# Optimization experiments

Hardware: AMD Instinct MI355X
Metric: run time of the kernel (lower is better)

The kernel has to match this reference:

```python
import jax, jax.numpy as jnp
import numpy as np

N, D, E, NNZ = 200000, 128, 1024, 1600000


def setup_inputs() -> dict:
    key = jax.random.key(0)
    ks = jax.random.split(key, 8)
    x = jax.random.normal(ks[0], (N, D), jnp.float32)
    tb_W = jax.random.normal(ks[1], (5, 3, D, D), jnp.float32) * 0.05
    tb_b = jax.random.normal(ks[2], (5, 3, D), jnp.float32) * 0.05
    hg_W = jax.random.normal(ks[3], (2, D, D), jnp.float32) * 0.05
    hg_b = jax.random.normal(ks[4], (2, D), jnp.float32) * 0.05
    hyperedge_attr = jax.random.normal(ks[5], (E, D), jnp.float32)
    node_idx = jax.random.randint(ks[6], (NNZ,), 0, N)
    edge_idx = jax.random.randint(ks[7], (NNZ,), 0, E)
    return dict(x=x, tb_W=tb_W, tb_b=tb_b, hg_W=hg_W, hg_b=hg_b,
                hyperedge_attr=hyperedge_attr, node_idx=node_idx,
                edge_idx=edge_idx, num_hyperedges=E)


def _time_block(x, W, b):
    # 1x1 Conv2d over channel dim == per-node linear. W:[3,D,D], b:[3,D]
    c1 = x @ W[0] + b[0]
    c2 = x @ W[1] + b[1]
    c3 = x @ W[2] + b[2]
    return jax.nn.relu(c1 + jax.nn.sigmoid(c2) + c3)


def _hypergraph_conv(x, node_idx, edge_idx, W, b, num_nodes, num_edges):
    # PyG HypergraphConv, use_attention=False (heads=1):
    # out = D^{-1} H B H^T (x W) + b, H given as COO (node_idx, edge_idx)
    xp = x @ W
    ones = jnp.ones(node_idx.shape[0], xp.dtype)
    Dn = jax.ops.segment_sum(ones, node_idx, num_segments=num_nodes)
    Dn = jnp.where(Dn > 0, 1.0 / Dn, 0.0)
    Be = jax.ops.segment_sum(ones, edge_idx, num_segments=num_edges)
    Be = jnp.where(Be > 0, 1.0 / Be, 0.0)
    # node -> hyperedge aggregation, normalized by 1/B_e
    m = jax.ops.segment_sum(xp[node_idx], edge_idx, num_segments=num_edges) * Be[:, None]
    # hyperedge -> node aggregation, normalized by 1/D_v
    out = jax.ops.segment_sum(m[edge_idx], node_idx, num_segments=num_nodes) * Dn[:, None]
    return out + b


def reference(x, tb_W, tb_b, hg_W, hg_b, hyperedge_attr, node_idx, edge_idx, num_hyperedges):
    # hyperedge_attr is unused when use_attention=False (faithful to PyG)
    n = x.shape[0]
    h = _time_block(x, tb_W[0], tb_b[0])
    h = _hypergraph_conv(h, node_idx, edge_idx, hg_W[0], hg_b[0], n, num_hyperedges)
    h = _time_block(h, tb_W[1], tb_b[1])
    h = _time_block(h, tb_W[2], tb_b[2])
    h = _hypergraph_conv(h, node_idx, edge_idx, hg_W[1], hg_b[1], n, num_hyperedges)
    h = _time_block(h, tb_W[3], tb_b[3])
    h = _time_block(h, tb_W[4], tb_b[4])
    return h
```

## Files before the change

kernel.cpp:

```cpp
#include <hip/hip_runtime.h>
#include <stdint.h>

#define N_NODES 200000
#define DIM     128
#define N_EDGES 1024
#define NNZ_C   1600000
#define NT64    3125

#define NBLK   250
#define CHUNK  6400
#define ITERS  25
#define NCB    196

#define NG_BLOCKS 2000
#define NG_WAVES  (NG_BLOCKS*4)
#define NG_K      25
#define NG_STAGE  512

typedef __attribute__((ext_vector_type(8))) short short8;
typedef __attribute__((ext_vector_type(4))) float f32x4;

__device__ __forceinline__ float u2f(uint32_t u){ union{uint32_t u;float f;} x; x.u=u; return x.f; }
__device__ __forceinline__ uint32_t f2u(float f){ union{uint32_t u;float f;} x; x.f=f; return x.u; }
__device__ __forceinline__ unsigned short f2bf(float f){
  uint32_t u = f2u(f);
  u += 0x7fffu + ((u >> 16) & 1u);
  return (unsigned short)(u >> 16);
}
__device__ __forceinline__ float fsig(float x){
  float e = __builtin_amdgcn_exp2f(x * -1.44269504088896340736f);
  return __builtin_amdgcn_rcpf(1.f + e);
}

__global__ void prep_tb_w(const float* __restrict__ W, short* __restrict__ Wt){
  int i = blockIdx.x*256 + threadIdx.x;
  if (i >= 5*256*128) return;
  int k   = i & 127;
  int col = (i >> 7) & 255;
  int s   = i >> 15;
  int j = col >> 7, n = col & 127;
  float v;
  if (j == 0)
    v = W[((s*3 + 0)*128 + k)*128 + n] + W[((s*3 + 2)*128 + k)*128 + n];
  else
    v = W[((s*3 + 1)*128 + k)*128 + n];
  Wt[i] = (short)f2bf(v);
}
__global__ void prep_hg_wf(const float* __restrict__ W, float* __restrict__ Wtf){
  int i = blockIdx.x*256 + threadIdx.x;
  if (i >= 2*128*128) return;
  int k = i & 127;
  int n = (i >> 7) & 127;
  int g = i >> 14;
  Wtf[i] = W[(g*128 + k)*128 + n];
}

__global__ __launch_bounds__(256) void hist_kernel(
    const int* __restrict__ nidx, const int* __restrict__ eidx,
    int* __restrict__ ebh, int* __restrict__ nbh)
{
  __shared__ int eh[N_EDGES];
  __shared__ int nh[NCB];
  int tid = threadIdx.x, blk = blockIdx.x;
  #pragma unroll
  for (int l = tid; l < N_EDGES; l += 256) eh[l] = 0;
  for (int l = tid; l < NCB; l += 256) nh[l] = 0;
  __syncthreads();
  int base = blk*CHUNK;
  for (int it = 0; it < ITERS; it++){
    int i = base + it*256 + tid;
    atomicAdd(&eh[eidx[i]], 1);
    atomicAdd(&nh[nidx[i] >> 10], 1);
  }
  __syncthreads();
  for (int l = tid; l < N_EDGES; l += 256) ebh[blk*N_EDGES + l] = eh[l];
  for (int l = tid; l < NCB; l += 256) nbh[blk*NCB + l] = nh[l];
}

__global__ __launch_bounds__(1024) void escan_kernel(
    int* __restrict__ ebh, int* __restrict__ eoff)
{
  __shared__ int sc[1024];
  int e = threadIdx.x;
  int total = 0;
  #pragma unroll 10
  for (int b = 0; b < NBLK; b++){
    int idx = b*N_EDGES + e;
    int t = ebh[idx];
    ebh[idx] = total;
    total += t;
  }
  sc[e] = total; __syncthreads();
  for (int off=1; off<1024; off<<=1){
    int v = (e >= off) ? sc[e-off] : 0;
    __syncthreads();
    sc[e] += v;
    __syncthreads();
  }
  int base = sc[e] - total;
  eoff[e] = base;
  if (e == 1023) eoff[1024] = sc[1023];
  #pragma unroll 10
  for (int b = 0; b < NBLK; b++) ebh[b*N_EDGES + e] += base;
}

__global__ __launch_bounds__(256) void nscan_kernel(
    int* __restrict__ nbh, int* __restrict__ cbase)
{
  __shared__ int sc[256];
  int c = threadIdx.x;
  int total = 0;
  if (c < NCB){
    #pragma unroll 10
    for (int b = 0; b < NBLK; b++){
      int idx = b*NCB + c;
      int t = nbh[idx];
      nbh[idx] = total;
      total += t;
    }
  }
  sc[c] = (c < NCB) ? total : 0; __syncthreads();
  for (int off=1; off<256; off<<=1){
    int v = (c >= off) ? sc[c-off] : 0;
    __syncthreads();
    sc[c] += v;
    __syncthreads();
  }
  int base = sc[c] - ((c < NCB) ? total : 0);
  if (c < NCB) cbase[c] = base;
  if (c == NCB-1) cbase[NCB] = sc[c];
  __syncthreads();
  if (c < NCB){
    #pragma unroll 10
    for (int b = 0; b < NBLK; b++) nbh[b*NCB + c] += base;
  }
}

__global__ __launch_bounds__(256) void scatter_kernel(
    const int* __restrict__ nidx, const int* __restrict__ eidx,
    const int* __restrict__ ebh, const int* __restrict__ nbh,
    int* __restrict__ enodes, uint32_t* __restrict__ pairs)
{
  __shared__ int cure[N_EDGES];
  __shared__ int curn[NCB];
  int tid = threadIdx.x, blk = blockIdx.x;
  for (int l = tid; l < N_EDGES; l += 256) cure[l] = ebh[blk*N_EDGES + l];
  for (int l = tid; l < NCB; l += 256)     curn[l] = nbh[blk*NCB + l];
  __syncthreads();
  int base = blk*CHUNK;
  for (int it = 0; it < ITERS; it++){
    int i = base + it*256 + tid;
    int v = nidx[i], e = eidx[i];
    int pe = atomicAdd(&cure[e], 1);
    enodes[pe] = v;
    int pn = atomicAdd(&curn[v >> 10], 1);
    pairs[pn] = ((uint32_t)v << 10) | (uint32_t)e;
  }
}

__global__ __launch_bounds__(256) void node_build_kernel(
    const uint32_t* __restrict__ pairs, const int* __restrict__ cbase,
    int* __restrict__ noff, int* __restrict__ nedges)
{
  __shared__ int cnt[1024];
  __shared__ int off[1024];
  __shared__ int part[256];
  int tid = threadIdx.x, c = blockIdx.x;
  int n0 = c << 10;
  int nloc = min(1024, N_NODES - n0);
  int s = cbase[c], e = cbase[c+1];
  #pragma unroll
  for (int l = tid; l < 1024; l += 256) cnt[l] = 0;
  __syncthreads();
  for (int i = s + tid; i < e; i += 256)
    atomicAdd(&cnt[(pairs[i] >> 10) & 1023], 1);
  __syncthreads();
  int c0 = cnt[tid*4], c1 = cnt[tid*4+1], c2 = cnt[tid*4+2], c3 = cnt[tid*4+3];
  int sum = c0+c1+c2+c3;
  part[tid] = sum; __syncthreads();
  for (int o=1; o<256; o<<=1){
    int v = (tid >= o) ? part[tid-o] : 0;
    __syncthreads();
    part[tid] += v;
    __syncthreads();
  }
  int pb = part[tid] - sum;
  off[tid*4]   = pb;
  off[tid*4+1] = pb + c0;
  off[tid*4+2] = pb + c0 + c1;
  off[tid*4+3] = pb + c0 + c1 + c2;
  __syncthreads();
  for (int l = tid; l < nloc; l += 256) noff[n0 + l] = s + off[l];
  if (c == 0 && tid == 0) noff[N_NODES] = NNZ_C;
  __syncthreads();
  for (int i = s + tid; i < e; i += 256){
    uint32_t p = pairs[i];
    int local = (p >> 10) & 1023;
    int pos = s + atomicAdd(&off[local], 1);
    nedges[pos] = (int)((p & 1023) << 8);
  }
}

template<bool IN_F32, int OUT_MODE>
__global__ __launch_bounds__(512, 6) void gemm_kernel(
    const void* __restrict__ in, void* __restrict__ out,
    const short* __restrict__ Wt, const float* __restrict__ bias)
{
  __shared__ short Atile[64][136];
  const int tid  = threadIdx.x;
  const int lane = tid & 63;
  const int w    = tid >> 6;
  const int l15  = lane & 15;
  const int quad = lane >> 4;
  const int ncol = w*16 + l15;

  short8 bfrag[2][4];
  #pragma unroll
  for (int j = 0; j < 2; j++){
    const short* bp = Wt + (j*128 + ncol)*128 + quad*8;
    #pragma unroll
    for (int ks = 0; ks < 4; ks++)
      bfrag[j][ks] = *(const short8*)(bp + ks*32);
  }
  float bv13 = bias[ncol] + bias[256 + ncol];
  float bv2  = bias[128 + ncol];

  const int arow = tid >> 4;
  const int aseg = tid & 15;

  short8 pre0, pre1;
  auto loadA = [&](int t){
    int off0 = (t*64 + arow)*128 + aseg*8;
    int off1 = off0 + 32*128;
    if (IN_F32){
      const float* f = (const float*)in;
      #pragma unroll
      for (int h = 0; h < 2; h++){
        const float* fp = f + (h ? off1 : off0);
        f32x4 q0 = *(const f32x4*)fp;
        f32x4 q1 = *(const f32x4*)(fp + 4);
        short8 t0;
        #pragma unroll
        for (int u = 0; u < 4; u++){
          t0[u]   = (short)f2bf(q0[u]);
          t0[u+4] = (short)f2bf(q1[u]);
        }
        if (h) pre1 = t0; else pre0 = t0;
      }
    } else {
      pre0 = *(const short8*)((const short*)in + off0);
      pre1 = *(const short8*)((const short*)in + off1);
    }
  };

  int t = blockIdx.x;
  loadA(t);
  for (;;){
    __syncthreads();
    *(short8*)&Atile[arow][aseg*8]      = pre0;
    *(short8*)&Atile[arow + 32][aseg*8] = pre1;
    __syncthreads();
    int tn = t + gridDim.x;
    if (tn < NT64) loadA(tn);

    const int base = t*64;
    #pragma unroll
    for (int rt = 0; rt < 4; rt++){
      short8 af[4];
      #pragma unroll
      for (int ks = 0; ks < 4; ks++)
        af[ks] = *(const short8*)&Atile[rt*16 + l15][ks*32 + quad*8];

      f32x4 acc[2];
      #pragma unroll
      for (int j = 0; j < 2; j++){
        acc[j] = (f32x4){0.f, 0.f, 0.f, 0.f};
        #pragma unroll
        for (int ks = 0; ks < 4; ks++)
          acc[j] = __builtin_amdgcn_mfma_f32_16x16x32_bf16(
              af[ks], bfrag[j][ks], acc[j], 0, 0, 0);
      }

      #pragma unroll
      for (int r = 0; r < 4; r++){
        int row = base + rt*16 + quad*4 + r;
        float sg = fsig(acc[1][r] + bv2);
        float v = acc[0][r] + bv13 + sg;
        v = fmaxf(v, 0.f);
        if (OUT_MODE == 1) ((float*)out)[row*128 + ncol] = v;
        else if (OUT_MODE == 0) ((unsigned short*)out)[row*128 + ncol] = f2bf(v);
        else {
          int pk = __builtin_amdgcn_cvt_pk_fp8_f32(v, v, 0, false);
          ((unsigned char*)out)[row*128 + ncol] = (unsigned char)(pk & 0xff);
        }
      }
    }
    if (tn >= NT64) break;
    t = tn;
  }
}

__device__ __forceinline__ void acc16(float* a, uint4 r){
  uint32_t w[4] = {r.x, r.y, r.z, r.w};
  #pragma unroll
  for (int q = 0; q < 4; q++){
    auto lo = __builtin_amdgcn_cvt_pk_f32_fp8(w[q], false);
    auto hi = __builtin_amdgcn_cvt_pk_f32_fp8(w[q], true);
    a[q*4+0] += lo[0]; a[q*4+1] += lo[1]; a[q*4+2] += hi[0]; a[q*4+3] += hi[1];
  }
}

__global__ __launch_bounds__(256) void edge_gather_kernel(
    const unsigned char* __restrict__ h8, const int* __restrict__ eoff,
    const int* __restrict__ enodes, float* __restrict__ s_e)
{
  int e = blockIdx.x;
  int s = eoff[e], en = eoff[e+1];
  int tid  = threadIdx.x;
  int slot = tid >> 3;
  int ch   = tid & 7;
  const size_t choff = (size_t)ch * 16;

  float a[16];
  #pragma unroll
  for (int j = 0; j < 16; j++) a[j] = 0.f;

  int i0 = s + slot;
  int n0 = (i0      < en) ? enodes[i0]      : -1;
  int n1 = (i0 + 32 < en) ? enodes[i0 + 32] : -1;
  int n2 = (i0 + 64 < en) ? enodes[i0 + 64] : -1;
  int n3 = (i0 + 96 < en) ? enodes[i0 + 96] : -1;

  while (i0 < en){
    int i1 = i0 + 128;
    int m0 = (i1      < en) ? enodes[i1]      : -1;
    int m1 = (i1 + 32 < en) ? enodes[i1 + 32] : -1;
    int m2 = (i1 + 64 < en) ? enodes[i1 + 64] : -1;
    int m3 = (i1 + 96 < en) ? enodes[i1 + 96] : -1;

    uint4 r0 = *(const uint4*)(h8 + (((size_t)max(n0,0)) << 7) + choff);
    uint4 r1 = *(const uint4*)(h8 + (((size_t)max(n1,0)) << 7) + choff);
    uint4 r2 = *(const uint4*)(h8 + (((size_t)max(n2,0)) << 7) + choff);
    uint4 r3 = *(const uint4*)(h8 + (((size_t)max(n3,0)) << 7) + choff);
    if (n0 < 0) r0 = make_uint4(0,0,0,0);
    if (n1 < 0) r1 = make_uint4(0,0,0,0);
    if (n2 < 0) r2 = make_uint4(0,0,0,0);
    if (n3 < 0) r3 = make_uint4(0,0,0,0);

    acc16(a, r0); acc16(a, r1); acc16(a, r2); acc16(a, r3);

    n0 = m0; n1 = m1; n2 = m2; n3 = m3;
    i0 = i1;
  }

  __shared__ float red[32][132];
  #pragma unroll
  for (int j = 0; j < 16; j++) red[slot][ch*16 + j] = a[j];
  __syncthreads();
  if (tid < 128){
    float sum = 0.f;
    #pragma unroll
    for (int r = 0; r < 32; r++) sum += red[r][tid];
    s_e[e*128 + tid] = sum;
  }
}

__global__ __launch_bounds__(128) void egemm_kernel(
    const float* __restrict__ s_e, const int* __restrict__ eoff,
    const float* __restrict__ Wtf, uint32_t* __restrict__ mbf)
{
  __shared__ float srow[128];
  __shared__ float sacc[128];
  int e = blockIdx.x, n = threadIdx.x;
  srow[n] = s_e[e*128 + n];
  __syncthreads();
  int deg = eoff[e+1] - eoff[e];
  float be = deg > 0 ? 1.f/(float)deg : 0.f;
  const f32x4* w4 = (const f32x4*)(Wtf + n*128);
  float acc = 0.f;
  #pragma unroll
  for (int k = 0; k < 32; k++){
    f32x4 qv = w4[k];
    acc += qv[0]*srow[k*4] + qv[1]*srow[k*4+1] + qv[2]*srow[k*4+2] + qv[3]*srow[k*4+3];
  }
  sacc[n] = acc * be;
  __syncthreads();
  if (n < 64){
    uint32_t lo = f2bf(sacc[2*n]);
    uint32_t hi = f2bf(sacc[2*n+1]);
    mbf[e*64 + n] = (hi << 16) | lo;
  }
}

__global__ __launch_bounds__(256) void node_gather_kernel(
    const uint32_t* __restrict__ mbf, const int* __restrict__ noff,
    const int* __restrict__ nedges, const float* __restrict__ hb,
    uint32_t* __restrict__ outp)
{
  __shared__ int sidx[4][NG_STAGE];
  const int wslot = threadIdx.x >> 6;
  const int wid   = (blockIdx.x << 2) | wslot;
  const int lane  = threadIdx.x & 63;
  const int lane4 = lane << 2;
  const float b0 = hb[2*lane], b1 = hb[2*lane+1];
  const int v0 = wid * NG_K;

  int eArr = noff[min(v0 + 1 + lane, N_NODES)];
  int sW   = __builtin_amdgcn_readfirstlane(noff[v0]);
  int send = __builtin_amdgcn_readlane(eArr, NG_K - 1);
  int n = send - sW;

  int* myIdx = sidx[wslot];
  bool useLds = (n <= NG_STAGE);
  if (useLds){
    for (int b = lane; b < n; b += 64) myIdx[b] = nedges[sW + b];
  }
  __syncthreads();

  const char* mb = (const char*)mbf;
  if (useLds){
    int s = sW;
    for (int vr = 0; vr < NG_K; vr++){
      int e = __builtin_amdgcn_readlane(eArr, vr);
      float a0 = 0.f, a1 = 0.f;
      uint32_t rlast = 0;
      for (int i = s; i < e; i += 8){
        uint32_t r[8];
        #pragma unroll
        for (int k = 0; k < 8; k++){
          int li = min(i + k, e - 1) - sW;
          r[k] = *(const uint32_t*)(mb + (myIdx[li] + lane4));
        }
        #pragma unroll
        for (int k = 0; k < 8; k++){
          a0 += u2f(r[k] << 16);
          a1 += u2f(r[k] & 0xffff0000u);
        }
        rlast = r[7];
      }
      int d = e - s;
      float dead = (float)(((d + 7) & ~7) - d);
      a0 -= dead * u2f(rlast << 16);
      a1 -= dead * u2f(rlast & 0xffff0000u);
      float dn = (d > 0) ? 1.f/(float)d : 0.f;
      uint32_t lo = f2bf(a0*dn + b0);
      uint32_t hi = f2bf(a1*dn + b1);
      outp[((size_t)(v0 + vr) << 6) | lane] = (hi << 16) | lo;
      s = e;
    }
  } else {
    int s = sW;
    for (int vr = 0; vr < NG_K; vr++){
      int e = __builtin_amdgcn_readlane(eArr, vr);
      float a0 = 0.f, a1 = 0.f;
      for (int i = s; i < e; i++){
        uint32_t r = *(const uint32_t*)(mb + (nedges[i] + lane4));
        a0 += u2f(r << 16);
        a1 += u2f(r & 0xffff0000u);
      }
      int d = e - s;
      float dn = (d > 0) ? 1.f/(float)d : 0.f;
      uint32_t lo = f2bf(a0*dn + b0);
      uint32_t hi = f2bf(a1*dn + b1);
      outp[((size_t)(v0 + vr) << 6) | lane] = (hi << 16) | lo;
      s = e;
    }
  }
}

extern "C" void kernel_launch(void* const* d_in, const int* in_sizes, int n_in,
                              void* d_out, int out_size, void* d_ws, size_t ws_size,
                              hipStream_t stream)
{
  (void)in_sizes; (void)n_in; (void)out_size; (void)ws_size;
  const float* x   = (const float*)d_in[0];
  const float* tbW = (const float*)d_in[1];
  const float* tbb = (const float*)d_in[2];
  const float* hgW = (const float*)d_in[3];
  const float* hgb = (const float*)d_in[4];
  const int* nidx  = (const int*)d_in[6];
  const int* eidx  = (const int*)d_in[7];
  float* out = (float*)d_out;

  char* p = (char*)d_ws;
  auto alloc = [&](size_t sz){ void* r = (void*)p; p += (sz + 255) & ~(size_t)255; return r; };
  unsigned short* hA = (unsigned short*)alloc((size_t)N_NODES*DIM*2);
  unsigned short* hB = (unsigned short*)alloc((size_t)N_NODES*DIM*2);
  unsigned char*  h8 = (unsigned char*)alloc((size_t)N_NODES*DIM);
  float* s_e  = (float*)alloc((size_t)N_EDGES*DIM*4);
  uint32_t* mbf = (uint32_t*)alloc((size_t)N_EDGES*64*4);
  short* WtTb = (short*)alloc((size_t)5*256*128*2);
  float* Wtf  = (float*)alloc((size_t)2*128*128*4);
  int* ebh  = (int*)alloc((size_t)NBLK*N_EDGES*4);
  int* nbh  = (int*)alloc((size_t)NBLK*NCB*4);
  int* eoff = (int*)alloc((N_EDGES+1)*4);
  int* cbase= (int*)alloc((NCB+1)*4);
  int* noff = (int*)alloc((size_t)(N_NODES+1)*4);
  int* enodes = (int*)alloc((size_t)NNZ_C*4);
  int* nedges = (int*)alloc((size_t)NNZ_C*4 + 64);
  uint32_t* pairs = (uint32_t*)h8;

  prep_tb_w<<<640, 256, 0, stream>>>(tbW, WtTb);
  prep_hg_wf<<<128, 256, 0, stream>>>(hgW, Wtf);

  hist_kernel<<<NBLK, 256, 0, stream>>>(nidx, eidx, ebh, nbh);
  escan_kernel<<<1, 1024, 0, stream>>>(ebh, eoff);
  nscan_kernel<<<1, 256, 0, stream>>>(nbh, cbase);
  scatter_kernel<<<NBLK, 256, 0, stream>>>(nidx, eidx, ebh, nbh, enodes, pairs);
  node_build_kernel<<<NCB, 256, 0, stream>>>(pairs, cbase, noff, nedges);

  gemm_kernel<true, 2><<<1250, 512, 0, stream>>>(x, h8, WtTb, tbb);
  edge_gather_kernel<<<N_EDGES, 256, 0, stream>>>(h8, eoff, enodes, s_e);
  egemm_kernel<<<N_EDGES, 128, 0, stream>>>(s_e, eoff, Wtf, mbf);
  node_gather_kernel<<<NG_BLOCKS, 256, 0, stream>>>(mbf, noff, nedges, hgb, (uint32_t*)hA);
  gemm_kernel<false, 0><<<1250, 512, 0, stream>>>(hA, hB, WtTb + 1*32768, tbb + 1*384);
  gemm_kernel<false, 2><<<1250, 512, 0, stream>>>(hB, h8, WtTb + 2*32768, tbb + 2*384);
  edge_gather_kernel<<<N_EDGES, 256, 0, stream>>>(h8, eoff, enodes, s_e);
  egemm_kernel<<<N_EDGES, 128, 0, stream>>>(s_e, eoff, Wtf + 16384, mbf);
  node_gather_kernel<<<NG_BLOCKS, 256, 0, stream>>>(mbf, noff, nedges, hgb + 128, (uint32_t*)hA);
  gemm_kernel<false, 0><<<1250, 512, 0, stream>>>(hA, hB, WtTb + 3*32768, tbb + 3*384);
  gemm_kernel<false, 1><<<1250, 512, 0, stream>>>(hB, out, WtTb + 4*32768, tbb + 4*384);
}
```

Baseline: 625.7 us.

## Fuse edge GEMM into edge gather, merge scans, double-buffer GEMM tile

Folds the per-hyperedge 128x128 projection into the edge gather kernel, which removes the s_e round trip through global memory and one launch per conv layer. Merges the edge and node prefix scans into a single two-block launch. Double-buffers the shared A tile in the node GEMM so one barrier per tile iteration can be dropped. The cost is double the GEMM LDS footprint, which could lower occupancy under the 6-block launch bound, and heavier edge-gather blocks.

```diff
diff --git a/kernel.cpp b/kernel.cpp
--- a/kernel.cpp
+++ b/kernel.cpp
@@ -77,62 +77,61 @@
   for (int l = tid; l < NCB; l += 256) nbh[blk*NCB + l] = nh[l];
 }
 
-__global__ __launch_bounds__(1024) void escan_kernel(
-    int* __restrict__ ebh, int* __restrict__ eoff)
+__global__ __launch_bounds__(1024) void scan_kernel(
+    int* __restrict__ ebh, int* __restrict__ eoff,
+    int* __restrict__ nbh, int* __restrict__ cbase)
 {
   __shared__ int sc[1024];
-  int e = threadIdx.x;
-  int total = 0;
-  #pragma unroll 10
-  for (int b = 0; b < NBLK; b++){
-    int idx = b*N_EDGES + e;
-    int t = ebh[idx];
-    ebh[idx] = total;
-    total += t;
-  }
-  sc[e] = total; __syncthreads();
-  for (int off=1; off<1024; off<<=1){
-    int v = (e >= off) ? sc[e-off] : 0;
-    __syncthreads();
-    sc[e] += v;
-    __syncthreads();
-  }
-  int base = sc[e] - total;
-  eoff[e] = base;
-  if (e == 1023) eoff[1024] = sc[1023];
-  #pragma unroll 10
-  for (int b = 0; b < NBLK; b++) ebh[b*N_EDGES + e] += base;
-}
-
-__global__ __launch_bounds__(256) void nscan_kernel(
-    int* __restrict__ nbh, int* __restrict__ cbase)
-{
-  __shared__ int sc[256];
-  int c = threadIdx.x;
-  int total = 0;
-  if (c < NCB){
+  int tid = threadIdx.x;
+  if (blockIdx.x == 0){
+    int e = tid;
+    int total = 0;
     #pragma unroll 10
     for (int b = 0; b < NBLK; b++){
-      int idx = b*NCB + c;
-      int t = nbh[idx];
-      nbh[idx] = total;
+      int idx = b*N_EDGES + e;
+      int t = ebh[idx];
+      ebh[idx] = total;
       total += t;
     }
-  }
-  sc[c] = (c < NCB) ? total : 0; __syncthreads();
-  for (int off=1; off<256; off<<=1){
-    int v = (c >= off) ? sc[c-off] : 0;
+    sc[e] = total; __syncthreads();
+    for (int off=1; off<1024; off<<=1){
+      int v = (e >= off) ? sc[e-off] : 0;
+      __syncthreads();
+      sc[e] += v;
+      __syncthreads();
+    }
+    int base = sc[e] - total;
+    eoff[e] = base;
+    if (e == 1023) eoff[1024] = sc[1023];
+    #pragma unroll 10
+    for (int b = 0; b < NBLK; b++) ebh[b*N_EDGES + e] += base;
+  } else {
+    int c = tid;
+    int total = 0;
+    if (c < NCB){
+      #pragma unroll 10
+      for (int b = 0; b < NBLK; b++){
+        int idx = b*NCB + c;
+        int t = nbh[idx];
+        nbh[idx] = total;
+        total += t;
+      }
+    }
+    if (c < 256) sc[c] = (c < NCB) ? total : 0;
     __syncthreads();
-    sc[c] += v;
-    __syncthreads();
-  }
-  int base = sc[c] - ((c < NCB) ? total : 0);
-  if (c < NCB) cbase[c] = base;
-  if (c == NCB-1) cbase[NCB] = sc[c];
-  __syncthreads();
-  if (c < NCB){
-    #pragma unroll 10
-    for (int b = 0; b < NBLK; b++) nbh[b*NCB + c] += base;
+    for (int off=1; off<256; off<<=1){
+      int v = (c < 256 && c >= off) ? sc[c-off] : 0;
+      __syncthreads();
+      if (c < 256) sc[c] += v;
+      __syncthreads();
+    }
+    if (c < NCB){
+      int base = sc[c] - total;
+      cbase[c] = base;
+      if (c == NCB-1) cbase[NCB] = sc[c];
+      #pragma unroll 10
+      for (int b = 0; b < NBLK; b++) nbh[b*NCB + c] += base;
+    }
   }
 }
 
@@ -206,7 +205,7 @@
     const void* __restrict__ in, void* __restrict__ out,
     const short* __restrict__ Wt, const float* __restrict__ bias)
 {
-  __shared__ short Atile[64][136];
+  __shared__ short Atile[2][64][136];
   const int tid  = threadIdx.x;
   const int lane = tid & 63;
   const int w    = tid >> 6;
@@ -254,11 +253,11 @@
   };
 
   int t = blockIdx.x;
+  int p = 0;
   loadA(t);
   for (;;){
-    __syncthreads();
-    *(short8*)&Atile[arow][aseg*8]      = pre0;
-    *(short8*)&Atile[arow + 32][aseg*8] = pre1;
+    *(short8*)&Atile[p][arow][aseg*8]      = pre0;
+    *(short8*)&Atile[p][arow + 32][aseg*8] = pre1;
     __syncthreads();
     int tn = t + gridDim.x;
     if (tn < NT64) loadA(tn);
@@ -269,7 +268,7 @@
       short8 af[4];
       #pragma unroll
       for (int ks = 0; ks < 4; ks++)
-        af[ks] = *(const short8*)&Atile[rt*16 + l15][ks*32 + quad*8];
+        af[ks] = *(const short8*)&Atile[p][rt*16 + l15][ks*32 + quad*8];
 
       f32x4 acc[2];
       #pragma unroll
@@ -297,6 +296,7 @@
     }
     if (tn >= NT64) break;
     t = tn;
+    p ^= 1;
   }
 }
 
@@ -312,7 +312,8 @@
 
 __global__ __launch_bounds__(256) void edge_gather_kernel(
     const unsigned char* __restrict__ h8, const int* __restrict__ eoff,
-    const int* __restrict__ enodes, float* __restrict__ s_e)
+    const int* __restrict__ enodes, const float* __restrict__ Wtf,
+    uint32_t* __restrict__ mbf)
 {
   int e = blockIdx.x;
   int s = eoff[e], en = eoff[e+1];
@@ -354,6 +355,8 @@
   }
 
   __shared__ float red[32][132];
+  __shared__ float srow[128];
+  __shared__ float sacc[128];
   #pragma unroll
   for (int j = 0; j < 16; j++) red[slot][ch*16 + j] = a[j];
   __syncthreads();
@@ -361,34 +364,26 @@
     float sum = 0.f;
     #pragma unroll
     for (int r = 0; r < 32; r++) sum += red[r][tid];
-    s_e[e*128 + tid] = sum;
-  }
-}
-
-__global__ __launch_bounds__(128) void egemm_kernel(
-    const float* __restrict__ s_e, const int* __restrict__ eoff,
-    const float* __restrict__ Wtf, uint32_t* __restrict__ mbf)
-{
-  __shared__ float srow[128];
-  __shared__ float sacc[128];
-  int e = blockIdx.x, n = threadIdx.x;
-  srow[n] = s_e[e*128 + n];
-  __syncthreads();
-  int deg = eoff[e+1] - eoff[e];
+    srow[tid] = sum;
+  }
+  __syncthreads();
+  int deg = en - s;
   float be = deg > 0 ? 1.f/(float)deg : 0.f;
-  const f32x4* w4 = (const f32x4*)(Wtf + n*128);
-  float acc = 0.f;
-  #pragma unroll
-  for (int k = 0; k < 32; k++){
-    f32x4 qv = w4[k];
-    acc += qv[0]*srow[k*4] + qv[1]*srow[k*4+1] + qv[2]*srow[k*4+2] + qv[3]*srow[k*4+3];
-  }
-  sacc[n] = acc * be;
-  __syncthreads();
-  if (n < 64){
-    uint32_t lo = f2bf(sacc[2*n]);
-    uint32_t hi = f2bf(sacc[2*n+1]);
-    mbf[e*64 + n] = (hi << 16) | lo;
+  if (tid < 128){
+    const f32x4* w4 = (const f32x4*)(Wtf + tid*128);
+    float acc = 0.f;
+    #pragma unroll
+    for (int k = 0; k < 32; k++){
+      f32x4 qv = w4[k];
+      acc += qv[0]*srow[k*4] + qv[1]*srow[k*4+1] + qv[2]*srow[k*4+2] + qv[3]*srow[k*4+3];
+    }
+    sacc[tid] = acc * be;
+  }
+  __syncthreads();
+  if (tid < 64){
+    uint32_t lo = f2bf(sacc[2*tid]);
+    uint32_t hi = f2bf(sacc[2*tid+1]);
+    mbf[e*64 + tid] = (hi << 16) | lo;
   }
 }
 
@@ -487,7 +482,6 @@
   unsigned short* hA = (unsigned short*)alloc((size_t)N_NODES*DIM*2);
   unsigned short* hB = (unsigned short*)alloc((size_t)N_NODES*DIM*2);
   unsigned char*  h8 = (unsigned char*)alloc((size_t)N_NODES*DIM);
-  float* s_e  = (float*)alloc((size_t)N_EDGES*DIM*4);
   uint32_t* mbf = (uint32_t*)alloc((size_t)N_EDGES*64*4);
   short* WtTb = (short*)alloc((size_t)5*256*128*2);
   float* Wtf  = (float*)alloc((size_t)2*128*128*4);
@@ -504,19 +498,16 @@
   prep_hg_wf<<<128, 256, 0, stream>>>(hgW, Wtf);
 
   hist_kernel<<<NBLK, 256, 0, stream>>>(nidx, eidx, ebh, nbh);
-  escan_kernel<<<1, 1024, 0, stream>>>(ebh, eoff);
-  nscan_kernel<<<1, 256, 0, stream>>>(nbh, cbase);
+  scan_kernel<<<2, 1024, 0, stream>>>(ebh, eoff, nbh, cbase);
   scatter_kernel<<<NBLK, 256, 0, stream>>>(nidx, eidx, ebh, nbh, enodes, pairs);
   node_build_kernel<<<NCB, 256, 0, stream>>>(pairs, cbase, noff, nedges);
 
   gemm_kernel<true, 2><<<1250, 512, 0, stream>>>(x, h8, WtTb, tbb);
-  edge_gather_kernel<<<N_EDGES, 256, 0, stream>>>(h8, eoff, enodes, s_e);
-  egemm_kernel<<<N_EDGES, 128, 0, stream>>>(s_e, eoff, Wtf, mbf);
+  edge_gather_kernel<<<N_EDGES, 256, 0, stream>>>(h8, eoff, enodes, Wtf, mbf);
   node_gather_kernel<<<NG_BLOCKS, 256, 0, stream>>>(mbf, noff, nedges, hgb, (uint32_t*)hA);
   gemm_kernel<false, 0><<<1250, 512, 0, stream>>>(hA, hB, WtTb + 1*32768, tbb + 1*384);
   gemm_kernel<false, 2><<<1250, 512, 0, stream>>>(hB, h8, WtTb + 2*32768, tbb + 2*384);
-  edge_gather_kernel<<<N_EDGES, 256, 0, stream>>>(h8, eoff, enodes, s_e);
-  egemm_kernel<<<N_EDGES, 128, 0, stream>>>(s_e, eoff, Wtf + 16384, mbf);
+  edge_gather_kernel<<<N_EDGES, 256, 0, stream>>>(h8, eoff, enodes, Wtf + 16384, mbf);
   node_gather_kernel<<<NG_BLOCKS, 256, 0, stream>>>(mbf, noff, nedges, hgb + 128, (uint32_t*)hA);
   gemm_kernel<false, 0><<<1250, 512, 0, stream>>>(hA, hB, WtTb + 3*32768, tbb + 3*384);
   gemm_kernel<false, 1><<<1250, 512, 0, stream>>>(hB, out, WtTb + 4*32768, tbb + 4*384);
```

Result: no change. 626.6 us (+0.2%).
